# Performance work log

Hardware: AMD Instinct MI355X
Metric: run time of the kernel (lower is better)

Reference implementation:

```python
import jax, jax.numpy as jnp
import numpy as np

B, N, D = 2, 16384, 512
H = 256          # gated-attention hidden dim
C, K = 4, 8      # num classes, descriptions per class
EPS = 1e-12


def _l2norm(x):
    return x / jnp.clip(jnp.linalg.norm(x, axis=-1, keepdims=True), EPS)


def setup_inputs() -> dict:
    key = jax.random.key(0)
    ks = jax.random.split(key, 12)
    inp = {
        'x_s': jax.random.normal(ks[0], (B, N, D), jnp.float32),
        'coord_s': jax.random.uniform(ks[1], (B, N, 2), jnp.float32),
        'x_l': jax.random.normal(ks[2], (B, N, D), jnp.float32),
        'coord_l': jax.random.uniform(ks[3], (B, N, 2), jnp.float32),
        # visual_proj: Linear(D, D), stored as [in, out] (apply x @ W + b)
        'W_proj': jax.random.normal(ks[4], (D, D), jnp.float32) / np.sqrt(D),
        'b_proj': jnp.zeros((D,), jnp.float32),
        # frozen, L2-normalized text description features [C, K, D]
        'desc_feats': _l2norm(jax.random.normal(ks[5], (C, K, D), jnp.float32)),
        # GatedAttentionPooling params ([in, out] layout)
        'Wv': jax.random.normal(ks[6], (D, H), jnp.float32) / np.sqrt(D),
        'bv': jnp.zeros((H,), jnp.float32),
        'Wu': jax.random.normal(ks[7], (D, H), jnp.float32) / np.sqrt(D),
        'bu': jnp.zeros((H,), jnp.float32),
        'w_attn': jax.random.normal(ks[8], (H,), jnp.float32) / np.sqrt(H),
        'b_attn': jnp.zeros((), jnp.float32),
    }
    return inp


def _class_scores(xp, desc_feats):
    # xp: [B,N,D] normalized projected patches; desc_feats: [C,K,D]
    scale = desc_feats.shape[-1] ** (-0.5)
    sim = jnp.einsum('bnd,ckd->bnck', xp, desc_feats) * scale  # [B,N,C,K]
    attn = jax.nn.softmax(sim, axis=-1)
    # scores_c = <xp, attn @ desc_c> collapsed without materializing [B,N,C,D]
    return jnp.einsum('bnck,ckd,bnd->bnc', attn, desc_feats, xp)  # [B,N,C]


def _gated_pool(feats, Wv, bv, Wu, bu, w_attn, b_attn):
    # feats: [B,N,D]
    A_V = jnp.tanh(feats @ Wv + bv)                 # [B,N,H]
    A_U = jax.nn.sigmoid(feats @ Wu + bu)           # [B,N,H]
    A = (A_V * A_U) @ w_attn + b_attn               # [B,N]
    A = jax.nn.softmax(A, axis=1)
    return jnp.einsum('bn,bnd->bd', A, feats)       # [B,D]


def reference(x_s, coord_s, x_l, coord_l, W_proj, b_proj, desc_feats,
              Wv, bv, Wu, bu, w_attn, b_attn):
    # coords are unused by the compute path (kept for signature fidelity)
    x_s_proj = _l2norm(_l2norm(x_s) @ W_proj + b_proj)
    x_l_proj = _l2norm(_l2norm(x_l) @ W_proj + b_proj)

    class_scores_s = _class_scores(x_s_proj, desc_feats)  # [B,N,C]
    class_scores_l = _class_scores(x_l_proj, desc_feats)

    slide_s = _l2norm(_gated_pool(x_s_proj, Wv, bv, Wu, bu, w_attn, b_attn))
    slide_l = _l2norm(_gated_pool(x_l_proj, Wv, bv, Wu, bu, w_attn, b_attn))

    # text_features_low: per-class max over descriptions, L2-normalized
    text_feats = _l2norm(jnp.max(desc_feats, axis=1))      # [C,D]

    logits = slide_s @ text_feats.T + slide_l @ text_feats.T  # [B,C]
    Y_prob = jax.nn.softmax(logits, axis=1)
    Y_hat = jnp.argmax(Y_prob, axis=1)
    return Y_prob, Y_hat, class_scores_s, class_scores_l
```

## Files before the change

kernel.cpp:

```cpp
#include <hip/hip_runtime.h>
#include <math.h>

#define B_ 2
#define N_ 16384
#define D_ 512
#define C_ 4
#define K_ 8
#define ROWS (B_*N_)
#define ROWS2 (2*ROWS)
#define EPS_ 1e-12f

typedef unsigned short u16;
typedef unsigned int u32;
using short8  = __attribute__((ext_vector_type(8))) short;
using float4v = __attribute__((ext_vector_type(4))) float;

__device__ __forceinline__ u16 f2bf(float f) {
    union { float f; u32 u; } v; v.f = f;
    u32 r = v.u + 0x7fffu + ((v.u >> 16) & 1u);
    return (u16)(r >> 16);
}
__device__ __forceinline__ u32 pack2(float a, float b) {
    return (u32)f2bf(a) | ((u32)f2bf(b) << 16);
}
__device__ __forceinline__ float bf2f(u16 h) {
    union { u32 u; float f; } v; v.u = ((u32)h) << 16;
    return v.f;
}
__device__ __forceinline__ float fsigmoid(float x) { return 1.0f / (1.0f + __expf(-x)); }
__device__ __forceinline__ float ftanh(float x)    { return 1.0f - 2.0f / (__expf(2.0f * x) + 1.0f); }

__device__ __forceinline__ void load_lds16(const u16* g, u16* l) {
    __builtin_amdgcn_global_load_lds(
        (const __attribute__((address_space(1))) u32*)g,
        (__attribute__((address_space(3))) u32*)l, 16, 0, 0);
}
__device__ __forceinline__ void stage_rows8(const u16* gtile, u16* ldsTile, int g, int lane) {
    int rg = lane >> 3;
    int c  = (lane & 7) ^ rg;
    load_lds16(gtile + (size_t)(g * 8 + rg) * 512 + c * 8, ldsTile + g * 512);
}
#define AFRAG(lds, R, c) (*(const short8*)&(lds)[(R) * 64 + (((c) ^ ((R) & 7)) * 8)])
#define BFRAG(Bf, nf, ks, lane) (*(const short8*)&(Bf)[((size_t)((nf) * 16 + (ks)) << 9) + ((lane) << 3)])

__global__ __launch_bounds__(256) void prep_weights_kernel(
    const float* __restrict__ Wp, const float* __restrict__ Wv, const float* __restrict__ Wu,
    const float* __restrict__ bv, const float* __restrict__ bu, const float* __restrict__ desc,
    u16* __restrict__ WpF, u16* __restrict__ WvuF, float* __restrict__ bvu,
    u16* __restrict__ descF)
{
    int idx = blockIdx.x * 256 + threadIdx.x;
    int e = idx & 7, l = (idx >> 3) & 63, ks = (idx >> 9) & 15, nf = idx >> 13;
    int k = ks * 32 + ((l >> 4) << 3) + e;
    int n = (nf << 4) + (l & 15);
    WpF[idx] = f2bf(Wp[(size_t)k * 512 + n]);
    int half = nf & 1, h = (nf >> 1) * 16 + (l & 15);
    WvuF[idx] = f2bf(half ? Wu[(size_t)k * 256 + h] : Wv[(size_t)k * 256 + h]);
    if (idx < 512) {
        int tl = idx >> 4, pr = tl >> 1, hf = tl & 1, hh = pr * 16 + (idx & 15);
        bvu[idx] = hf ? bu[hh] : bv[hh];
    }
    if (idx < 16384) {
        int j = idx & 7, dl = (idx >> 3) & 63, g = (idx >> 9) & 1, kt = idx >> 10;
        descF[idx] = f2bf(desc[(size_t)(g * 16 + (dl & 15)) * 512 + kt * 32 + (dl >> 4) * 8 + j]);
    }
}

__global__ __launch_bounds__(256) void rownorm_cast_kernel(
    const float* __restrict__ x_s, const float* __restrict__ x_l, u16* __restrict__ xn)
{
    int wave = threadIdx.x >> 6, lane = threadIdx.x & 63;
    size_t row = (size_t)blockIdx.x * 4 + wave;
    const float* xr = (row < (size_t)ROWS) ? (x_s + row * D_)
                                           : (x_l + (row - ROWS) * D_);
    float4 a = *(const float4*)&xr[lane * 8];
    float4 b = *(const float4*)&xr[lane * 8 + 4];
    float s = a.x*a.x + a.y*a.y + a.z*a.z + a.w*a.w
            + b.x*b.x + b.y*b.y + b.z*b.z + b.w*b.w;
#pragma unroll
    for (int off = 32; off; off >>= 1) s += __shfl_xor(s, off, 64);
    float inv = 1.0f / fmaxf(sqrtf(s), EPS_);
    uint4 o;
    o.x = pack2(a.x * inv, a.y * inv);
    o.y = pack2(a.z * inv, a.w * inv);
    o.z = pack2(b.x * inv, b.y * inv);
    o.w = pack2(b.z * inv, b.w * inv);
    *(uint4*)&xn[row * D_ + lane * 8] = o;
}

__device__ __forceinline__ void decode_mn(int d, int& M0, int& N0) {
    int n = (d >> 3) & 3;
    int m = (d & 7) | ((d >> 5) << 3);
    M0 = m * 128; N0 = n * 128;
}

__global__ __launch_bounds__(256, 2) void gemm_bias_kernel(
    const u16* __restrict__ A, const u16* __restrict__ Bf,
    const float* __restrict__ bias, u16* __restrict__ C, float* __restrict__ sumsq)
{
    __shared__ u16 ldsA[2][128 * 64];
    int t = threadIdx.x, wave = t >> 6, lane = t & 63;
    int lr = lane & 15, lq = lane >> 4;
    int wm = wave >> 1, wn = wave & 1;
    int M0, N0; decode_mn(blockIdx.x, M0, N0);
    const u16* Arow = A + (size_t)M0 * 512;

    float4v acc[4][4];
#pragma unroll
    for (int i = 0; i < 4; ++i)
#pragma unroll
        for (int j = 0; j < 4; ++j)
#pragma unroll
            for (int r = 0; r < 4; ++r) acc[i][j][r] = 0.f;

#pragma unroll
    for (int s = 0; s < 4; ++s) stage_rows8(Arow, ldsA[0], wave * 4 + s, lane);
    __syncthreads();

    for (int tt = 0; tt < 8; ++tt) {
        int cur = tt & 1;
        if (tt < 7) {
            const u16* Ab = Arow + (tt + 1) * 64;
#pragma unroll
            for (int s = 0; s < 4; ++s) stage_rows8(Ab, ldsA[cur ^ 1], wave * 4 + s, lane);
        }
#pragma unroll
        for (int kt = 0; kt < 2; ++kt) {
            int ks = tt * 2 + kt;
            short8 af[4], bfr[4];
#pragma unroll
            for (int i = 0; i < 4; ++i)
                af[i] = AFRAG(ldsA[cur], wm * 64 + i * 16 + lr, kt * 4 + lq);
#pragma unroll
            for (int j = 0; j < 4; ++j)
                bfr[j] = BFRAG(Bf, (N0 >> 4) + wn * 4 + j, ks, lane);
#pragma unroll
            for (int i = 0; i < 4; ++i)
#pragma unroll
                for (int j = 0; j < 4; ++j)
                    acc[i][j] = __builtin_amdgcn_mfma_f32_16x16x32_bf16(bfr[j], af[i], acc[i][j], 0, 0, 0);
        }
        __syncthreads();
    }

    float4 b4[4];
#pragma unroll
    for (int j = 0; j < 4; ++j)
        b4[j] = *(const float4*)&bias[N0 + wn * 64 + j * 16 + lq * 4];
#pragma unroll
    for (int i = 0; i < 4; ++i) {
        int m = M0 + wm * 64 + i * 16 + lr;
        u16* crow = C + (size_t)m * 512;
        float sq = 0.f;
#pragma unroll
        for (int j = 0; j < 4; ++j) {
            int nb = N0 + wn * 64 + j * 16 + lq * 4;
            float v0 = acc[i][j][0] + b4[j].x, v1 = acc[i][j][1] + b4[j].y;
            float v2 = acc[i][j][2] + b4[j].z, v3 = acc[i][j][3] + b4[j].w;
            u16 h0 = f2bf(v0), h1 = f2bf(v1), h2 = f2bf(v2), h3 = f2bf(v3);
            uint2 o;
            o.x = (u32)h0 | ((u32)h1 << 16);
            o.y = (u32)h2 | ((u32)h3 << 16);
            *(uint2*)&crow[nb] = o;
            float q0 = bf2f(h0), q1 = bf2f(h1), q2 = bf2f(h2), q3 = bf2f(h3);
            sq += q0*q0 + q1*q1 + q2*q2 + q3*q3;
        }
        sq += __shfl_xor(sq, 16, 64);
        sq += __shfl_xor(sq, 32, 64);
        if (lq == 0) atomicAdd(&sumsq[m], sq);
    }
}

__global__ __launch_bounds__(256, 2) void gatecls_kernel(
    const u16* __restrict__ A, const u16* __restrict__ Bf,
    const u16* __restrict__ descF,
    const float* __restrict__ bvu, const float* __restrict__ w_attn,
    const float* __restrict__ sumsq, float* __restrict__ Araw4,
    float* __restrict__ out10)
{
    __shared__ u16 ldsA[2][128 * 64];
    int t = threadIdx.x, wave = t >> 6, lane = t & 63;
    int lr = lane & 15, lq = lane >> 4;
    int wm = wave >> 1, wn = wave & 1;
    int M0, N0; decode_mn(blockIdx.x, M0, N0);
    const int nblk = (N0 >> 7);
    const bool doCls = (nblk == 0);
    const u16* Arow = A + (size_t)M0 * 512;

    float4v acc[4][4];
    float4v accS[2][2];
#pragma unroll
    for (int i = 0; i < 4; ++i)
#pragma unroll
        for (int j = 0; j < 4; ++j)
#pragma unroll
            for (int r = 0; r < 4; ++r) acc[i][j][r] = 0.f;
#pragma unroll
    for (int h = 0; h < 2; ++h)
#pragma unroll
        for (int r = 0; r < 4; ++r) { accS[h][0][r] = 0.f; accS[h][1][r] = 0.f; }

#pragma unroll
    for (int s = 0; s < 4; ++s) stage_rows8(Arow, ldsA[0], wave * 4 + s, lane);
    __syncthreads();

    for (int tt = 0; tt < 8; ++tt) {
        int cur = tt & 1;
        if (tt < 7) {
            const u16* Ab = Arow + (tt + 1) * 64;
#pragma unroll
            for (int s = 0; s < 4; ++s) stage_rows8(Ab, ldsA[cur ^ 1], wave * 4 + s, lane);
        }
#pragma unroll
        for (int kt = 0; kt < 2; ++kt) {
            int ks = tt * 2 + kt;
            if (doCls) {
                short8 d0 = *(const short8*)&descF[(ks * 2 + 0) * 512 + lane * 8];
                short8 d1 = *(const short8*)&descF[(ks * 2 + 1) * 512 + lane * 8];
#pragma unroll
                for (int h = 0; h < 2; ++h) {
                    short8 afc = AFRAG(ldsA[cur], wave * 32 + h * 16 + lr, kt * 4 + lq);
                    accS[h][0] = __builtin_amdgcn_mfma_f32_16x16x32_bf16(afc, d0, accS[h][0], 0, 0, 0);
                    accS[h][1] = __builtin_amdgcn_mfma_f32_16x16x32_bf16(afc, d1, accS[h][1], 0, 0, 0);
                }
            }
            short8 af[4], bfr[4];
#pragma unroll
            for (int i = 0; i < 4; ++i)
                af[i] = AFRAG(ldsA[cur], wm * 64 + i * 16 + lr, kt * 4 + lq);
#pragma unroll
            for (int j = 0; j < 4; ++j)
                bfr[j] = BFRAG(Bf, (N0 >> 4) + wn * 4 + j, ks, lane);
#pragma unroll
            for (int i = 0; i < 4; ++i)
#pragma unroll
                for (int j = 0; j < 4; ++j)
                    acc[i][j] = __builtin_amdgcn_mfma_f32_16x16x32_bf16(bfr[j], af[i], acc[i][j], 0, 0, 0);
        }
        __syncthreads();
    }

    if (doCls) {
        const float scale = 0.04419417382415922f;
        int side = (M0 >= ROWS) ? 1 : 0;
        float* cls = out10 + (size_t)side * ((size_t)ROWS * 4);
#pragma unroll
        for (int h = 0; h < 2; ++h) {
#pragma unroll
            for (int r = 0; r < 4; ++r) {
                int grow = M0 + wave * 32 + h * 16 + lq * 4 + r;
                float iv = 1.0f / fmaxf(sqrtf(sumsq[grow]), EPS_);
                float sv0 = accS[h][0][r] * iv, sv1 = accS[h][1][r] * iv;
#pragma unroll
                for (int g = 0; g < 2; ++g) {
                    float s = g ? sv1 : sv0;
                    float ts = s * scale;
                    float mx = ts;
                    mx = fmaxf(mx, __shfl_xor(mx, 1, 64));
                    mx = fmaxf(mx, __shfl_xor(mx, 2, 64));
                    mx = fmaxf(mx, __shfl_xor(mx, 4, 64));
                    float e = __expf(ts - mx);
                    float num = e * s, den = e;
                    num += __shfl_xor(num, 1, 64); den += __shfl_xor(den, 1, 64);
                    num += __shfl_xor(num, 2, 64); den += __shfl_xor(den, 2, 64);
                    num += __shfl_xor(num, 4, 64); den += __shfl_xor(den, 4, 64);
                    if ((lr & 7) == 0) {
                        int c = g * 2 + ((lr >> 3) & 1);
                        cls[(size_t)(grow - side * ROWS) * 4 + c] = num / den;
                    }
                }
            }
        }
    }

    int colbase = N0 + wn * 64;
    int hbase = colbase >> 1;
    float4 bv4[2], bu4[2], w4[2];
#pragma unroll
    for (int p = 0; p < 2; ++p) {
        int nv = colbase + p * 32 + lq * 4;
        bv4[p] = *(const float4*)&bvu[nv];
        bu4[p] = *(const float4*)&bvu[nv + 16];
        w4[p]  = *(const float4*)&w_attn[hbase + p * 16 + lq * 4];
    }
    float* redA = (float*)&ldsA[0][0];
#pragma unroll
    for (int i = 0; i < 4; ++i) {
        int rloc = wm * 64 + i * 16 + lr;
        float iv = 1.0f / fmaxf(sqrtf(sumsq[M0 + rloc]), EPS_);
        float part = 0.f;
#pragma unroll
        for (int p = 0; p < 2; ++p) {
#pragma unroll
            for (int r = 0; r < 4; ++r) {
                float v = acc[i][2 * p][r] * iv + (&bv4[p].x)[r];
                float u = acc[i][2 * p + 1][r] * iv + (&bu4[p].x)[r];
                part += ftanh(v) * (&w4[p].x)[r] * fsigmoid(u);
            }
        }
        part += __shfl_xor(part, 16, 64);
        part += __shfl_xor(part, 32, 64);
        if (lq == 0) redA[wn * 128 + rloc] = part;
    }
    __syncthreads();
    if (t < 128)
        Araw4[(size_t)nblk * ROWS2 + M0 + t] = redA[t] + redA[128 + t];
}

__global__ __launch_bounds__(256) void areduce_kernel(
    float* __restrict__ Araw4, float* __restrict__ part)
{
    __shared__ float red[256];
    int t = threadIdx.x, g = blockIdx.y;
    size_t i0 = (size_t)g * N_ + blockIdx.x * 512 + t * 2;
    float v0 = Araw4[i0]     + Araw4[i0 + ROWS2]     + Araw4[i0 + 2*ROWS2]     + Araw4[i0 + 3*ROWS2];
    float v1 = Araw4[i0 + 1] + Araw4[i0 + 1 + ROWS2] + Araw4[i0 + 1 + 2*ROWS2] + Araw4[i0 + 1 + 3*ROWS2];
    *(float2*)&Araw4[i0] = make_float2(v0, v1);
    red[t] = fmaxf(v0, v1); __syncthreads();
    for (int s = 128; s; s >>= 1) { if (t < s) red[t] = fmaxf(red[t], red[t + s]); __syncthreads(); }
    float m = red[0]; __syncthreads();
    red[t] = __expf(v0 - m) + __expf(v1 - m); __syncthreads();
    for (int s = 128; s; s >>= 1) { if (t < s) red[t] += red[t + s]; __syncthreads(); }
    if (t == 0) {
        int pi = g * 32 + blockIdx.x;
        part[pi * 2] = m;
        part[pi * 2 + 1] = red[0];
    }
}

__global__ __launch_bounds__(128) void acombine_kernel(
    const float* __restrict__ part, float* __restrict__ mg)
{
    int t = threadIdx.x;
    int g = t >> 5, j = t & 31;
    float m = part[(g * 32 + j) * 2];
    float s = part[(g * 32 + j) * 2 + 1];
    float mm = m;
#pragma unroll
    for (int off = 1; off < 32; off <<= 1) mm = fmaxf(mm, __shfl_xor(mm, off, 64));
    float sc = s * __expf(m - mm);
#pragma unroll
    for (int off = 1; off < 32; off <<= 1) sc += __shfl_xor(sc, off, 64);
    if (j == 0) {
        mg[g * 2] = mm;
        mg[g * 2 + 1] = 1.0f / sc;
    }
}

__global__ __launch_bounds__(256) void pool_kernel(
    const float* __restrict__ Araw, const float* __restrict__ sumsq,
    const float* __restrict__ mg, const u16* __restrict__ xpraw,
    float* __restrict__ slideAll)
{
    __shared__ float lds[4][512];
    int t = threadIdx.x, wave = t >> 6, lane = t & 63;
    int g = blockIdx.y;
    float m = mg[g * 2], is = mg[g * 2 + 1];
    size_t row0 = (size_t)g * N_ + (size_t)blockIdx.x * 256 + wave;
    float a[8] = {};
    for (int r = 0; r < 64; ++r) {
        size_t row = row0 + r * 4;
        float iv = 1.0f / fmaxf(sqrtf(sumsq[row]), EPS_);
        float av = __expf(Araw[row] - m) * is * iv;
        uint4 pk = *(const uint4*)&xpraw[row * D_ + lane * 8];
        a[0] += av * bf2f((u16)pk.x); a[1] += av * bf2f((u16)(pk.x >> 16));
        a[2] += av * bf2f((u16)pk.y); a[3] += av * bf2f((u16)(pk.y >> 16));
        a[4] += av * bf2f((u16)pk.z); a[5] += av * bf2f((u16)(pk.z >> 16));
        a[6] += av * bf2f((u16)pk.w); a[7] += av * bf2f((u16)(pk.w >> 16));
    }
#pragma unroll
    for (int i = 0; i < 8; ++i) lds[wave][lane * 8 + i] = a[i];
    __syncthreads();
#pragma unroll
    for (int q = 0; q < 2; ++q) {
        int c = t * 2 + q;
        float s = lds[0][c] + lds[1][c] + lds[2][c] + lds[3][c];
        atomicAdd(&slideAll[(size_t)g * 512 + c], s);
    }
}

__global__ __launch_bounds__(512) void finalize_kernel(
    const float* __restrict__ slide_s, const float* __restrict__ slide_l,
    const float* __restrict__ desc, float* __restrict__ out)
{
    __shared__ float txt[4][512];
    __shared__ float ssn[2][512];
    __shared__ float sln[2][512];
    __shared__ float red[512];
    __shared__ float lg[8];
    int t = threadIdx.x;

    auto reduceSum = [&](float v) -> float {
        red[t] = v; __syncthreads();
        for (int s = 256; s; s >>= 1) { if (t < s) red[t] += red[t + s]; __syncthreads(); }
        float r = red[0]; __syncthreads();
        return r;
    };

    for (int c = 0; c < 4; ++c) {
        float m = -1e30f;
        for (int k = 0; k < 8; ++k) m = fmaxf(m, desc[((size_t)c * 8 + k) * 512 + t]);
        float ss = reduceSum(m * m);
        txt[c][t] = m / fmaxf(sqrtf(ss), EPS_);
    }
    for (int b = 0; b < 2; ++b) {
        float v = slide_s[b * 512 + t];
        float ss = reduceSum(v * v);
        ssn[b][t] = v / fmaxf(sqrtf(ss), EPS_);
        v = slide_l[b * 512 + t];
        ss = reduceSum(v * v);
        sln[b][t] = v / fmaxf(sqrtf(ss), EPS_);
    }
    __syncthreads();
    for (int b = 0; b < 2; ++b)
        for (int c = 0; c < 4; ++c) {
            float v = ssn[b][t] * txt[c][t] + sln[b][t] * txt[c][t];
            float s = reduceSum(v);
            if (t == 0) lg[b * 4 + c] = s;
        }
    __syncthreads();
    if (t < 2) {
        int b = t;
        float m = -1e30f;
        for (int c = 0; c < 4; ++c) m = fmaxf(m, lg[b * 4 + c]);
        float e[4]; float den = 0.f;
        for (int c = 0; c < 4; ++c) { e[c] = expf(lg[b * 4 + c] - m); den += e[c]; }
        int am = 0; float bm = -1.f;
        for (int c = 0; c < 4; ++c) {
            float pcl = e[c] / den;
            out[b * 4 + c] = pcl;
            if (pcl > bm) { bm = pcl; am = c; }
        }
        out[8 + b] = (float)am;
    }
}

extern "C" void kernel_launch(void* const* d_in, const int* in_sizes, int n_in,
                              void* d_out, int out_size, void* d_ws, size_t ws_size,
                              hipStream_t stream) {
    const float* x_s    = (const float*)d_in[0];
    const float* x_l    = (const float*)d_in[2];
    const float* W_proj = (const float*)d_in[4];
    const float* b_proj = (const float*)d_in[5];
    const float* desc   = (const float*)d_in[6];
    const float* Wv     = (const float*)d_in[7];
    const float* bv     = (const float*)d_in[8];
    const float* Wu     = (const float*)d_in[9];
    const float* bu     = (const float*)d_in[10];
    const float* w_attn = (const float*)d_in[11];
    float* out = (float*)d_out;

    char* w = (char*)d_ws;
    u16* xn        = (u16*)w;
    u16* xpraw     = (u16*)(w + 67108864);
    u16* WpF       = (u16*)(w + 134217728);
    u16* WvuF      = (u16*)(w + 134742016);
    u16* descF     = (u16*)(w + 135266304);
    float* bvu     = (float*)(w + 135299072);
    float* sumsq   = (float*)(w + 135301120);
    float* slideAll= (float*)(w + 135563264);
    float* Araw4   = (float*)(w + 135571456);
    float* part    = (float*)(w + 136620032);
    float* mg      = (float*)(w + 136621056);

    hipMemsetAsync(sumsq, 0, 262144 + 8192, stream);
    prep_weights_kernel<<<1024, 256, 0, stream>>>(W_proj, Wv, Wu, bv, bu, desc,
                                                  WpF, WvuF, bvu, descF);

    rownorm_cast_kernel<<<ROWS2 / 4, 256, 0, stream>>>(x_s, x_l, xn);
    gemm_bias_kernel<<<2048, 256, 0, stream>>>(xn, WpF, b_proj, xpraw, sumsq);
    gatecls_kernel<<<2048, 256, 0, stream>>>(xpraw, WvuF, descF, bvu, w_attn,
                                             sumsq, Araw4, out + 10);
    areduce_kernel<<<dim3(32, 4), 256, 0, stream>>>(Araw4, part);
    acombine_kernel<<<1, 128, 0, stream>>>(part, mg);
    pool_kernel<<<dim3(64, 4), 256, 0, stream>>>(Araw4, sumsq, mg, xpraw, slideAll);
    finalize_kernel<<<1, 512, 0, stream>>>(slideAll, slideAll + 1024, desc, out);
}
```

Measured before the change: 341.3 us.

## Stage B weight fragments and desc tiles through LDS with async global_load_lds

Both GEMM kernels previously read the pre-swizzled B-weight fragments (and desc features) directly from global memory per MFMA step. They now double-buffer those tiles in LDS using global_load_lds, alongside the existing A staging, so the two waves that share each B fragment read it from LDS. The aim is to cut redundant global/L2 traffic and hide load latency behind compute. The cost is doubling the A-only LDS footprint (plus desc buffers), which may limit the two-blocks-per-CU occupancy target.

```diff
diff --git a/kernel.cpp b/kernel.cpp
--- a/kernel.cpp
+++ b/kernel.cpp
@@ -40,8 +40,10 @@
     int c  = (lane & 7) ^ rg;
     load_lds16(gtile + (size_t)(g * 8 + rg) * 512 + c * 8, ldsTile + g * 512);
 }
+__device__ __forceinline__ void stage_lin512(const u16* gsrc, u16* ldst, int lane) {
+    load_lds16(gsrc + lane * 8, ldst);
+}
 #define AFRAG(lds, R, c) (*(const short8*)&(lds)[(R) * 64 + (((c) ^ ((R) & 7)) * 8)])
-#define BFRAG(Bf, nf, ks, lane) (*(const short8*)&(Bf)[((size_t)((nf) * 16 + (ks)) << 9) + ((lane) << 3)])
 
 __global__ __launch_bounds__(256) void prep_weights_kernel(
     const float* __restrict__ Wp, const float* __restrict__ Wv, const float* __restrict__ Wu,
@@ -99,11 +101,13 @@
     const float* __restrict__ bias, u16* __restrict__ C, float* __restrict__ sumsq)
 {
     __shared__ u16 ldsA[2][128 * 64];
+    __shared__ u16 ldsB[2][128 * 64];
     int t = threadIdx.x, wave = t >> 6, lane = t & 63;
     int lr = lane & 15, lq = lane >> 4;
     int wm = wave >> 1, wn = wave & 1;
     int M0, N0; decode_mn(blockIdx.x, M0, N0);
-    const u16* Arow = A + (size_t)M0 * 512;
+    const u16* Arow  = A  + (size_t)M0 * 512;
+    const u16* Bbase = Bf + (size_t)(N0 >> 4) * 8192;
 
     float4v acc[4][4];
 #pragma unroll
@@ -115,6 +119,12 @@
 
 #pragma unroll
     for (int s = 0; s < 4; ++s) stage_rows8(Arow, ldsA[0], wave * 4 + s, lane);
+#pragma unroll
+    for (int s = 0; s < 4; ++s) {
+        int gp = wave * 4 + s;
+        stage_lin512(Bbase + (size_t)(gp >> 1) * 8192 + (gp & 1) * 512,
+                     ldsB[0] + gp * 512, lane);
+    }
     __syncthreads();
 
     for (int tt = 0; tt < 8; ++tt) {
@@ -123,17 +133,22 @@
             const u16* Ab = Arow + (tt + 1) * 64;
 #pragma unroll
             for (int s = 0; s < 4; ++s) stage_rows8(Ab, ldsA[cur ^ 1], wave * 4 + s, lane);
+#pragma unroll
+            for (int s = 0; s < 4; ++s) {
+                int gp = wave * 4 + s;
+                stage_lin512(Bbase + (size_t)(gp >> 1) * 8192 + (2 * (tt + 1) + (gp & 1)) * 512,
+                             ldsB[cur ^ 1] + gp * 512, lane);
+            }
         }
 #pragma unroll
         for (int kt = 0; kt < 2; ++kt) {
-            int ks = tt * 2 + kt;
             short8 af[4], bfr[4];
 #pragma unroll
             for (int i = 0; i < 4; ++i)
                 af[i] = AFRAG(ldsA[cur], wm * 64 + i * 16 + lr, kt * 4 + lq);
 #pragma unroll
             for (int j = 0; j < 4; ++j)
-                bfr[j] = BFRAG(Bf, (N0 >> 4) + wn * 4 + j, ks, lane);
+                bfr[j] = *(const short8*)&ldsB[cur][((wn * 4 + j) * 2 + kt) * 512 + lane * 8];
 #pragma unroll
             for (int i = 0; i < 4; ++i)
 #pragma unroll
@@ -179,13 +194,16 @@
     float* __restrict__ out10)
 {
     __shared__ u16 ldsA[2][128 * 64];
+    __shared__ u16 ldsB[2][128 * 64];
+    __shared__ u16 ldsD[2][2048];
     int t = threadIdx.x, wave = t >> 6, lane = t & 63;
     int lr = lane & 15, lq = lane >> 4;
     int wm = wave >> 1, wn = wave & 1;
     int M0, N0; decode_mn(blockIdx.x, M0, N0);
     const int nblk = (N0 >> 7);
     const bool doCls = (nblk == 0);
-    const u16* Arow = A + (size_t)M0 * 512;
+    const u16* Arow  = A  + (size_t)M0 * 512;
+    const u16* Bbase = Bf + (size_t)(N0 >> 4) * 8192;
 
     float4v acc[4][4];
     float4v accS[2][2];
@@ -202,6 +220,13 @@
 
 #pragma unroll
     for (int s = 0; s < 4; ++s) stage_rows8(Arow, ldsA[0], wave * 4 + s, lane);
+#pragma unroll
+    for (int s = 0; s < 4; ++s) {
+        int gp = wave * 4 + s;
+        stage_lin512(Bbase + (size_t)(gp >> 1) * 8192 + (gp & 1) * 512,
+                     ldsB[0] + gp * 512, lane);
+    }
+    if (doCls) stage_lin512(descF + wave * 512, ldsD[0] + wave * 512, lane);
     __syncthreads();
 
     for (int tt = 0; tt < 8; ++tt) {
@@ -210,13 +235,21 @@
             const u16* Ab = Arow + (tt + 1) * 64;
 #pragma unroll
             for (int s = 0; s < 4; ++s) stage_rows8(Ab, ldsA[cur ^ 1], wave * 4 + s, lane);
+#pragma unroll
+            for (int s = 0; s < 4; ++s) {
+                int gp = wave * 4 + s;
+                stage_lin512(Bbase + (size_t)(gp >> 1) * 8192 + (2 * (tt + 1) + (gp & 1)) * 512,
+                             ldsB[cur ^ 1] + gp * 512, lane);
+            }
+            if (doCls)
+                stage_lin512(descF + (tt + 1) * 2048 + wave * 512,
+                             ldsD[cur ^ 1] + wave * 512, lane);
         }
 #pragma unroll
         for (int kt = 0; kt < 2; ++kt) {
-            int ks = tt * 2 + kt;
             if (doCls) {
-                short8 d0 = *(const short8*)&descF[(ks * 2 + 0) * 512 + lane * 8];
-                short8 d1 = *(const short8*)&descF[(ks * 2 + 1) * 512 + lane * 8];
+                short8 d0 = *(const short8*)&ldsD[cur][(kt * 2 + 0) * 512 + lane * 8];
+                short8 d1 = *(const short8*)&ldsD[cur][(kt * 2 + 1) * 512 + lane * 8];
 #pragma unroll
                 for (int h = 0; h < 2; ++h) {
                     short8 afc = AFRAG(ldsA[cur], wave * 32 + h * 16 + lr, kt * 4 + lq);
@@ -230,7 +263,7 @@
                 af[i] = AFRAG(ldsA[cur], wm * 64 + i * 16 + lr, kt * 4 + lq);
 #pragma unroll
             for (int j = 0; j < 4; ++j)
-                bfr[j] = BFRAG(Bf, (N0 >> 4) + wn * 4 + j, ks, lane);
+                bfr[j] = *(const short8*)&ldsB[cur][((wn * 4 + j) * 2 + kt) * 512 + lane * 8];
 #pragma unroll
             for (int i = 0; i < 4; ++i)
 #pragma unroll
```

After: 347.5 us. No clear change (+1.8%).

## Triple-buffer A tiles in LDS and prefetch B fragments in registers

Applied to the files above, without the earlier changes.

Both MFMA GEMM kernels now use three LDS buffers for the A tile and two register sets for B-weight fragments (and desc fragments in the classifier path). Loads run two K-steps ahead of compute. Explicit s_waitcnt vmcnt values plus raw barriers replace __syncthreads, so only the oldest tile's loads must finish before each step. This is meant to hide global-load latency behind MFMA work, at the cost of more LDS per block and higher register pressure, which could spill or reduce occupancy.

```diff
diff --git a/kernel.cpp b/kernel.cpp
--- a/kernel.cpp
+++ b/kernel.cpp
@@ -42,6 +42,10 @@
 }
 #define AFRAG(lds, R, c) (*(const short8*)&(lds)[(R) * 64 + (((c) ^ ((R) & 7)) * 8)])
 #define BFRAG(Bf, nf, ks, lane) (*(const short8*)&(Bf)[((size_t)((nf) * 16 + (ks)) << 9) + ((lane) << 3)])
+
+#define WAITV4 asm volatile("s_waitcnt vmcnt(4)" ::: "memory")
+#define WAITV0 asm volatile("s_waitcnt vmcnt(0)" ::: "memory")
+#define BAR __builtin_amdgcn_s_barrier()
 
 __global__ __launch_bounds__(256) void prep_weights_kernel(
     const float* __restrict__ Wp, const float* __restrict__ Wv, const float* __restrict__ Wu,
@@ -94,16 +98,43 @@
     M0 = m * 128; N0 = n * 128;
 }
 
+#define STAGEA(ptr, ttv) \
+    { _Pragma("unroll") \
+      for (int s_ = 0; s_ < 4; ++s_) \
+          stage_rows8(Arow + (ttv) * 64, (ptr), wave * 4 + s_, lane); }
+
+#define LOADB(dst, ttv) \
+    { _Pragma("unroll") \
+      for (int j_ = 0; j_ < 4; ++j_) { \
+          dst[j_]     = BFRAG(Bf, nfb + j_, (ttv) * 2 + 0, lane); \
+          dst[4 + j_] = BFRAG(Bf, nfb + j_, (ttv) * 2 + 1, lane); \
+      } }
+
+#define GCOMP(PC, BR) \
+    { _Pragma("unroll") \
+      for (int kt = 0; kt < 2; ++kt) { \
+          short8 af[4]; \
+          _Pragma("unroll") \
+          for (int i_ = 0; i_ < 4; ++i_) \
+              af[i_] = AFRAG(PC, wm * 64 + i_ * 16 + lr, kt * 4 + lq); \
+          _Pragma("unroll") \
+          for (int i_ = 0; i_ < 4; ++i_) \
+              _Pragma("unroll") \
+              for (int j_ = 0; j_ < 4; ++j_) \
+                  acc[i_][j_] = __builtin_amdgcn_mfma_f32_16x16x32_bf16(BR[kt * 4 + j_], af[i_], acc[i_][j_], 0, 0, 0); \
+      } }
+
 __global__ __launch_bounds__(256, 2) void gemm_bias_kernel(
     const u16* __restrict__ A, const u16* __restrict__ Bf,
     const float* __restrict__ bias, u16* __restrict__ C, float* __restrict__ sumsq)
 {
-    __shared__ u16 ldsA[2][128 * 64];
+    __shared__ u16 ldsA[3][128 * 64];
     int t = threadIdx.x, wave = t >> 6, lane = t & 63;
     int lr = lane & 15, lq = lane >> 4;
     int wm = wave >> 1, wn = wave & 1;
     int M0, N0; decode_mn(blockIdx.x, M0, N0);
     const u16* Arow = A + (size_t)M0 * 512;
+    const int nfb = (N0 >> 4) + wn * 4;
 
     float4v acc[4][4];
 #pragma unroll
@@ -113,35 +144,30 @@
 #pragma unroll
             for (int r = 0; r < 4; ++r) acc[i][j][r] = 0.f;
 
-#pragma unroll
-    for (int s = 0; s < 4; ++s) stage_rows8(Arow, ldsA[0], wave * 4 + s, lane);
-    __syncthreads();
-
-    for (int tt = 0; tt < 8; ++tt) {
-        int cur = tt & 1;
-        if (tt < 7) {
-            const u16* Ab = Arow + (tt + 1) * 64;
-#pragma unroll
-            for (int s = 0; s < 4; ++s) stage_rows8(Ab, ldsA[cur ^ 1], wave * 4 + s, lane);
-        }
-#pragma unroll
-        for (int kt = 0; kt < 2; ++kt) {
-            int ks = tt * 2 + kt;
-            short8 af[4], bfr[4];
-#pragma unroll
-            for (int i = 0; i < 4; ++i)
-                af[i] = AFRAG(ldsA[cur], wm * 64 + i * 16 + lr, kt * 4 + lq);
-#pragma unroll
-            for (int j = 0; j < 4; ++j)
-                bfr[j] = BFRAG(Bf, (N0 >> 4) + wn * 4 + j, ks, lane);
-#pragma unroll
-            for (int i = 0; i < 4; ++i)
-#pragma unroll
-                for (int j = 0; j < 4; ++j)
-                    acc[i][j] = __builtin_amdgcn_mfma_f32_16x16x32_bf16(bfr[j], af[i], acc[i][j], 0, 0, 0);
-        }
-        __syncthreads();
-    }
+    short8 bA[8], bB[8];
+    u16 *p0 = &ldsA[0][0], *p1 = &ldsA[1][0], *p2 = &ldsA[2][0];
+
+    STAGEA(p0, 0);
+    LOADB(bA, 0);
+    STAGEA(p1, 1);
+    WAITV0; BAR;
+
+    for (int t2 = 0; t2 < 3; ++t2) {
+        int tt = t2 * 2;
+        LOADB(bB, tt + 1);
+        STAGEA(p2, tt + 2);
+        GCOMP(p0, bA);
+        WAITV4; BAR;
+        LOADB(bA, tt + 2);
+        STAGEA(p0, tt + 3);
+        GCOMP(p1, bB);
+        WAITV4; BAR;
+        u16* q0 = p0; u16* q1 = p1; p0 = p2; p1 = q0; p2 = q1;
+    }
+    LOADB(bB, 7);
+    GCOMP(p0, bA);
+    WAITV0; BAR;
+    GCOMP(p1, bB);
 
     float4 b4[4];
 #pragma unroll
@@ -171,6 +197,35 @@
     }
 }
 
+#define LOADD(dst, ttv) \
+    { _Pragma("unroll") \
+      for (int kt_ = 0; kt_ < 2; ++kt_) \
+          _Pragma("unroll") \
+          for (int g_ = 0; g_ < 2; ++g_) \
+              dst[kt_ * 2 + g_] = *(const short8*)&descF[((((ttv) * 2 + kt_) * 2 + g_) << 9) + (lane << 3)]; }
+
+#define GCOMPC(PC, BR, DR) \
+    { _Pragma("unroll") \
+      for (int kt = 0; kt < 2; ++kt) { \
+          if (doCls) { \
+              _Pragma("unroll") \
+              for (int h_ = 0; h_ < 2; ++h_) { \
+                  short8 afc = AFRAG(PC, wave * 32 + h_ * 16 + lr, kt * 4 + lq); \
+                  accS[h_][0] = __builtin_amdgcn_mfma_f32_16x16x32_bf16(afc, DR[kt * 2 + 0], accS[h_][0], 0, 0, 0); \
+                  accS[h_][1] = __builtin_amdgcn_mfma_f32_16x16x32_bf16(afc, DR[kt * 2 + 1], accS[h_][1], 0, 0, 0); \
+              } \
+          } \
+          short8 af[4]; \
+          _Pragma("unroll") \
+          for (int i_ = 0; i_ < 4; ++i_) \
+              af[i_] = AFRAG(PC, wm * 64 + i_ * 16 + lr, kt * 4 + lq); \
+          _Pragma("unroll") \
+          for (int i_ = 0; i_ < 4; ++i_) \
+              _Pragma("unroll") \
+              for (int j_ = 0; j_ < 4; ++j_) \
+                  acc[i_][j_] = __builtin_amdgcn_mfma_f32_16x16x32_bf16(BR[kt * 4 + j_], af[i_], acc[i_][j_], 0, 0, 0); \
+      } }
+
 __global__ __launch_bounds__(256, 2) void gatecls_kernel(
     const u16* __restrict__ A, const u16* __restrict__ Bf,
     const u16* __restrict__ descF,
@@ -178,7 +233,7 @@
     const float* __restrict__ sumsq, float* __restrict__ Araw4,
     float* __restrict__ out10)
 {
-    __shared__ u16 ldsA[2][128 * 64];
+    __shared__ u16 ldsA[3][128 * 64];
     int t = threadIdx.x, wave = t >> 6, lane = t & 63;
     int lr = lane & 15, lq = lane >> 4;
     int wm = wave >> 1, wn = wave & 1;
@@ -186,6 +241,7 @@
     const int nblk = (N0 >> 7);
     const bool doCls = (nblk == 0);
     const u16* Arow = A + (size_t)M0 * 512;
+    const int nfb = (N0 >> 4) + wn * 4;
 
     float4v acc[4][4];
     float4v accS[2][2];
@@ -200,45 +256,35 @@
 #pragma unroll
         for (int r = 0; r < 4; ++r) { accS[h][0][r] = 0.f; accS[h][1][r] = 0.f; }
 
-#pragma unroll
-    for (int s = 0; s < 4; ++s) stage_rows8(Arow, ldsA[0], wave * 4 + s, lane);
-    __syncthreads();
-
-    for (int tt = 0; tt < 8; ++tt) {
-        int cur = tt & 1;
-        if (tt < 7) {
-            const u16* Ab = Arow + (tt + 1) * 64;
-#pragma unroll
-            for (int s = 0; s < 4; ++s) stage_rows8(Ab, ldsA[cur ^ 1], wave * 4 + s, lane);
-        }
-#pragma unroll
-        for (int kt = 0; kt < 2; ++kt) {
-            int ks = tt * 2 + kt;
-            if (doCls) {
-                short8 d0 = *(const short8*)&descF[(ks * 2 + 0) * 512 + lane * 8];
-                short8 d1 = *(const short8*)&descF[(ks * 2 + 1) * 512 + lane * 8];
-#pragma unroll
-                for (int h = 0; h < 2; ++h) {
-                    short8 afc = AFRAG(ldsA[cur], wave * 32 + h * 16 + lr, kt * 4 + lq);
-                    accS[h][0] = __builtin_amdgcn_mfma_f32_16x16x32_bf16(afc, d0, accS[h][0], 0, 0, 0);
-                    accS[h][1] = __builtin_amdgcn_mfma_f32_16x16x32_bf16(afc, d1, accS[h][1], 0, 0, 0);
-                }
-            }
-            short8 af[4], bfr[4];
-#pragma unroll
-            for (int i = 0; i < 4; ++i)
-                af[i] = AFRAG(ldsA[cur], wm * 64 + i * 16 + lr, kt * 4 + lq);
-#pragma unroll
-            for (int j = 0; j < 4; ++j)
-                bfr[j] = BFRAG(Bf, (N0 >> 4) + wn * 4 + j, ks, lane);
-#pragma unroll
-            for (int i = 0; i < 4; ++i)
-#pragma unroll
-                for (int j = 0; j < 4; ++j)
-                    acc[i][j] = __builtin_amdgcn_mfma_f32_16x16x32_bf16(bfr[j], af[i], acc[i][j], 0, 0, 0);
-        }
-        __syncthreads();
-    }
+    short8 bA[8], bB[8];
+    short8 dA[4], dB[4];
+    u16 *p0 = &ldsA[0][0], *p1 = &ldsA[1][0], *p2 = &ldsA[2][0];
+
+    STAGEA(p0, 0);
+    LOADB(bA, 0);
+    if (doCls) LOADD(dA, 0);
+    STAGEA(p1, 1);
+    WAITV0; BAR;
+
+    for (int t2 = 0; t2 < 3; ++t2) {
+        int tt = t2 * 2;
+        LOADB(bB, tt + 1);
+        if (doCls) LOADD(dB, tt + 1);
+        STAGEA(p2, tt + 2);
+        GCOMPC(p0, bA, dA);
+        WAITV4; BAR;
+        LOADB(bA, tt + 2);
+        if (doCls) LOADD(dA, tt + 2);
+        STAGEA(p0, tt + 3);
+        GCOMPC(p1, bB, dB);
+        WAITV4; BAR;
+        u16* q0 = p0; u16* q1 = p1; p0 = p2; p1 = q0; p2 = q1;
+    }
+    LOADB(bB, 7);
+    if (doCls) LOADD(dB, 7);
+    GCOMPC(p0, bA, dA);
+    WAITV0; BAR;
+    GCOMPC(p1, bB, dB);
 
     if (doCls) {
         const float scale = 0.04419417382415922f;
```

Measured after the change: 361.8 us. +6.0%, slower.
